# Kernel tuning notes

Measured on AMD Instinct MI355X. Metric: run time of the kernel, lower is better.

Reference implementation:

```python
import jax, jax.numpy as jnp
import numpy as np

GRID_SIZE = 5
SPLINE_ORDER = 3
INPUT_DIM = 4096
BATCH = 4096
N_BASIS = GRID_SIZE + SPLINE_ORDER - 1  # 7


def _extended_knots():
    # Uniform grid on [-1, 1] extended by spline_order knots on each side so the
    # Cox-de Boor recursion is well defined (the original torch code indexes
    # grid[i+k+1] past the end; this is the standard intended knot extension).
    grid = np.linspace(-1.0, 1.0, GRID_SIZE)
    h = grid[1] - grid[0]
    left = grid[0] - h * np.arange(SPLINE_ORDER, 0, -1)
    right = grid[-1] + h * np.arange(1, SPLINE_ORDER + 1)
    return jnp.asarray(np.concatenate([left, grid, right]), dtype=jnp.float32)  # (11,)


def _bspline_basis(x, knots):
    # x: (B, D) -> basis: (B, D, N_BASIS), fully vectorized Cox-de Boor recursion.
    t = knots
    xe = x[..., None]                                   # (B, D, 1)
    Bk = ((xe >= t[:-1]) & (xe < t[1:])).astype(x.dtype)  # degree 0: (B, D, 10)
    for k in range(1, SPLINE_ORDER + 1):
        n = t.shape[0] - k - 1
        left = (xe - t[:n]) / (t[k:k + n] - t[:n]) * Bk[..., :n]
        right = (t[k + 1:k + 1 + n] - xe) / (t[k + 1:k + 1 + n] - t[1:1 + n]) * Bk[..., 1:n + 1]
        Bk = left + right
    return Bk  # (B, D, 7)


def setup_inputs() -> dict:
    key = jax.random.key(0)
    kx, kc = jax.random.split(key)
    x = jax.random.uniform(kx, (BATCH, INPUT_DIM), dtype=jnp.float32, minval=-1.0, maxval=1.0)
    coeffs = jax.random.normal(kc, (INPUT_DIM, N_BASIS), dtype=jnp.float32)
    return {"x": x, "coeffs": coeffs}


def reference(x, coeffs):
    knots = _extended_knots()
    basis = _bspline_basis(x, knots)          # (B, D, K)
    return jnp.einsum('bdk,dk->bd', basis, coeffs)
```

## Files before the change

### kernel.cpp

```cpp
#include <hip/hip_runtime.h>


typedef float f4v __attribute__((ext_vector_type(4)));

#define D     4096
#define B     4096
#define NB    7
#define DTILE 256
#define ROWS  32

constexpr int NDT    = D / DTILE;
constexpr int NRT    = B / ROWS;
constexpr int STRIDE = 20;

__global__ __launch_bounds__(256, 8) void
spline_act_kernel(const float* __restrict__ x,
                  const float* __restrict__ coeffs,
                  float* __restrict__ out) {
    __shared__ float sc[DTILE * STRIDE];

    const int bid   = blockIdx.x;
    const int dt    = bid & (NDT - 1);
    const int rowt  = bid >> 4;
    const int dbase = dt * DTILE;
    const int t     = threadIdx.x;

    {
        const f4v* c4 = reinterpret_cast<const f4v*>(coeffs + (size_t)dbase * NB);
        f4v* r4 = reinterpret_cast<f4v*>(sc);
        r4[t] = c4[t];
        if (t < (DTILE * NB / 4) - 256)
            r4[256 + t] = c4[256 + t];
        __syncthreads();

        const int dl = 4 * (t & 63) + (t >> 6);
        float cr[NB];
#pragma unroll
        for (int k = 0; k < NB; ++k) cr[k] = sc[dl * NB + k];
        __syncthreads();

        const float k6 = 1.0f / 6.0f;
        float* bp = &sc[t * STRIDE];
#pragma unroll
        for (int c = 0; c < 4; ++c) {
            float A  = cr[c];
            float Bv = cr[c + 1];
            float C  = cr[c + 2];
            float Dv = cr[c + 3];
            f4v p;
            p[0] = (A + 4.0f * Bv + C) * k6;
            p[1] = (C - A) * 0.5f;
            p[2] = (A + C) * 0.5f - Bv;
            p[3] = (Dv - A + 3.0f * (Bv - C)) * k6;
            *reinterpret_cast<f4v*>(bp + 4 * c) = p;
        }
        __syncthreads();
    }

    const int pos   = t & 63;
    const int rsub  = t >> 6;
    const int lbase = pos * STRIDE;

    const f4v* x4 = reinterpret_cast<const f4v*>(x);
    f4v*       o4 = reinterpret_cast<f4v*>(out);

    const int rowbase = rowt * ROWS;

#pragma unroll
    for (int it = 0; it < ROWS / 4; ++it) {
        const int row = rowbase + it * 4 + rsub;
        const int idx = row * (D / 4) + (dbase >> 2) + pos;

        const f4v xv = x4[idx];
        f4v r;
#pragma unroll
        for (int j = 0; j < 4; ++j) {
            float u  = fmaf(xv[j], 2.0f, 2.0f);
            float cf = floorf(u);
            cf = fminf(fmaxf(cf, 0.0f), 3.0f);
            float s  = u - cf;
            int   c  = (int)cf;
            const f4v cv = *reinterpret_cast<const f4v*>(
                &sc[lbase + j * (64 * STRIDE) + (c << 2)]);
            r[j] = fmaf(fmaf(fmaf(cv[3], s, cv[2]), s, cv[1]), s, cv[0]);
        }
        o4[idx] = r;
    }
}

extern "C" void kernel_launch(void* const* d_in, const int* in_sizes, int n_in,
                              void* d_out, int out_size, void* d_ws, size_t ws_size,
                              hipStream_t stream) {
    const float* x      = (const float*)d_in[0];
    const float* coeffs = (const float*)d_in[1];
    float* out          = (float*)d_out;

    const int grid = NDT * NRT;
    spline_act_kernel<<<grid, 256, 0, stream>>>(x, coeffs, out);
}
```

Measured before the change: 116.8 us.

## Drop shared-memory polynomial table; select coefficients from registers with select chains

Removes the per-block shared-memory staging of coefficients and the precomputed cubic polynomial table. Each thread now loads its 28 coefficients straight from global memory into registers and picks the four active ones with nested selects. It then evaluates the uniform cubic B-spline weights explicitly. It also halves ROWS, which doubles the grid, and limits unrolling to 2. This removes the LDS traffic and the barriers, at the cost of more ALU work per element and more register pressure.

```diff
diff --git a/kernel.cpp b/kernel.cpp
--- a/kernel.cpp
+++ b/kernel.cpp
@@ -7,66 +7,42 @@
 #define B     4096
 #define NB    7
 #define DTILE 256
-#define ROWS  32
+#define ROWS  16
 
-constexpr int NDT    = D / DTILE;
-constexpr int NRT    = B / ROWS;
-constexpr int STRIDE = 20;
+constexpr int NDT = D / DTILE;
+constexpr int NRT = B / ROWS;
 
 __global__ __launch_bounds__(256, 8) void
 spline_act_kernel(const float* __restrict__ x,
                   const float* __restrict__ coeffs,
                   float* __restrict__ out) {
-    __shared__ float sc[DTILE * STRIDE];
-
     const int bid   = blockIdx.x;
     const int dt    = bid & (NDT - 1);
     const int rowt  = bid >> 4;
     const int dbase = dt * DTILE;
     const int t     = threadIdx.x;
-
-    {
-        const f4v* c4 = reinterpret_cast<const f4v*>(coeffs + (size_t)dbase * NB);
-        f4v* r4 = reinterpret_cast<f4v*>(sc);
-        r4[t] = c4[t];
-        if (t < (DTILE * NB / 4) - 256)
-            r4[256 + t] = c4[256 + t];
-        __syncthreads();
-
-        const int dl = 4 * (t & 63) + (t >> 6);
-        float cr[NB];
-#pragma unroll
-        for (int k = 0; k < NB; ++k) cr[k] = sc[dl * NB + k];
-        __syncthreads();
-
-        const float k6 = 1.0f / 6.0f;
-        float* bp = &sc[t * STRIDE];
-#pragma unroll
-        for (int c = 0; c < 4; ++c) {
-            float A  = cr[c];
-            float Bv = cr[c + 1];
-            float C  = cr[c + 2];
-            float Dv = cr[c + 3];
-            f4v p;
-            p[0] = (A + 4.0f * Bv + C) * k6;
-            p[1] = (C - A) * 0.5f;
-            p[2] = (A + C) * 0.5f - Bv;
-            p[3] = (Dv - A + 3.0f * (Bv - C)) * k6;
-            *reinterpret_cast<f4v*>(bp + 4 * c) = p;
-        }
-        __syncthreads();
-    }
-
     const int pos   = t & 63;
     const int rsub  = t >> 6;
-    const int lbase = pos * STRIDE;
+
+    const f4v* c4 = reinterpret_cast<const f4v*>(
+        coeffs + (size_t)(dbase + 4 * pos) * NB);
+    const f4v q0 = c4[0], q1 = c4[1], q2 = c4[2], q3 = c4[3],
+              q4 = c4[4], q5 = c4[5], q6 = c4[6];
+
+    const float cr[4][NB] = {
+        {q0[0], q0[1], q0[2], q0[3], q1[0], q1[1], q1[2]},
+        {q1[3], q2[0], q2[1], q2[2], q2[3], q3[0], q3[1]},
+        {q3[2], q3[3], q4[0], q4[1], q4[2], q4[3], q5[0]},
+        {q5[1], q5[2], q5[3], q6[0], q6[1], q6[2], q6[3]},
+    };
 
     const f4v* x4 = reinterpret_cast<const f4v*>(x);
     f4v*       o4 = reinterpret_cast<f4v*>(out);
 
     const int rowbase = rowt * ROWS;
+    const float k6 = 1.0f / 6.0f;
 
-#pragma unroll
+#pragma unroll 2
     for (int it = 0; it < ROWS / 4; ++it) {
         const int row = rowbase + it * 4 + rsub;
         const int idx = row * (D / 4) + (dbase >> 2) + pos;
@@ -78,11 +54,27 @@
             float u  = fmaf(xv[j], 2.0f, 2.0f);
             float cf = floorf(u);
             cf = fminf(fmaxf(cf, 0.0f), 3.0f);
-            float s  = u - cf;
-            int   c  = (int)cf;
-            const f4v cv = *reinterpret_cast<const f4v*>(
-                &sc[lbase + j * (64 * STRIDE) + (c << 2)]);
-            r[j] = fmaf(fmaf(fmaf(cv[3], s, cv[2]), s, cv[1]), s, cv[0]);
+            const float s = u - cf;
+
+            const float* C = cr[j];
+            const bool b0 = cf < 0.5f;
+            const bool b1 = cf < 1.5f;
+            const bool b2 = cf < 2.5f;
+            const float t0 = b1 ? (b0 ? C[0] : C[1]) : (b2 ? C[2] : C[3]);
+            const float t1 = b1 ? (b0 ? C[1] : C[2]) : (b2 ? C[3] : C[4]);
+            const float t2 = b1 ? (b0 ? C[2] : C[3]) : (b2 ? C[4] : C[5]);
+            const float t3 = b1 ? (b0 ? C[3] : C[4]) : (b2 ? C[5] : C[6]);
+
+            const float omt = 1.0f - s;
+            const float s2  = s * s;
+            const float s3  = s2 * s;
+            const float w0 = omt * omt * omt * k6;
+            const float w1 = fmaf(3.0f, s3, fmaf(-6.0f, s2, 4.0f)) * k6;
+            const float w2 = fmaf(-3.0f, s3,
+                             fmaf(3.0f, s2, fmaf(3.0f, s, 1.0f))) * k6;
+            const float w3 = s3 * k6;
+
+            r[j] = fmaf(w0, t0, fmaf(w1, t1, fmaf(w2, t2, w3 * t3)));
         }
         o4[idx] = r;
     }
```

Measured after the change: 114.3 us. -2.2%, faster.
